# Kernel optimization log

Measured on AMD Instinct MI355X. Metric: run time of the kernel, lower is better.

Reference implementation:

```python
import jax, jax.numpy as jnp
import numpy as np

N = 50000      # nodes
E = 800000     # edges (avg degree 16)
C_IN = 64
C_OUT = 64
H = 32         # hidden_nf (hard-coded in module)
L = 4          # egnn_clean.EGNN default n_layers


def _lin(key, fan_in, fan_out):
    s = 1.0 / np.sqrt(fan_in)
    kw, kb = jax.random.split(key)
    w = jax.random.uniform(kw, (fan_in, fan_out), jnp.float32, -s, s)
    b = jax.random.uniform(kb, (fan_out,), jnp.float32, -s, s)
    return w, b


def _stack(key, fan_in, fan_out):
    ws, bs = zip(*[_lin(jax.random.fold_in(key, l), fan_in, fan_out) for l in range(L)])
    return jnp.stack(ws), jnp.stack(bs)


def setup_inputs() -> dict:
    key = jax.random.key(0)
    k = jax.random.split(key, 16)
    inp = {
        'data': jax.random.normal(k[0], (N, C_IN), jnp.float32),
        'pos': jax.random.normal(k[1], (N, 2), jnp.float32),
        'edge_attr': jax.random.normal(k[2], (E, 1), jnp.float32),
        't': jnp.ones((1,), jnp.float32),
        'row': jax.random.randint(k[3], (E,), 0, N),
        'col': jax.random.randint(k[4], (E,), 0, N),
    }
    inp['emb_in_w'], inp['emb_in_b'] = _lin(k[5], C_IN + 1, H)
    inp['emb_out_w'], inp['emb_out_b'] = _lin(k[6], H, C_OUT)
    inp['edge_w1'], inp['edge_b1'] = _stack(k[7], 2 * H + 2, H)  # [h_i, h_j, radial, edge_attr]
    inp['edge_w2'], inp['edge_b2'] = _stack(k[8], H, H)
    inp['node_w1'], inp['node_b1'] = _stack(k[9], 2 * H, H)
    inp['node_w2'], inp['node_b2'] = _stack(k[10], H, H)
    inp['coord_w1'], inp['coord_b1'] = _stack(k[11], H, H)
    lim = 0.001 * np.sqrt(6.0 / (H + 1))  # xavier_uniform gain=0.001, no bias
    inp['coord_w2'] = jax.random.uniform(k[12], (L, H, 1), jnp.float32, -lim, lim)
    return inp


def _egnn(data, pos, edge_attr, t, emb_in_w, emb_in_b, edge_w1, edge_b1, edge_w2, edge_b2,
          node_w1, node_b1, node_w2, node_b2, coord_w1, coord_b1, coord_w2,
          emb_out_w, emb_out_b, row, col):
    n = data.shape[0]
    silu = jax.nn.silu
    # prepend time channel; pad 2D coords with a zero z-column
    h = jnp.concatenate([jnp.broadcast_to(t.reshape(1, 1), (n, 1)), data], axis=1)  # [N, C_IN+1]
    x = jnp.concatenate([pos, jnp.zeros((n, 1), pos.dtype)], axis=1)                # [N, 3]
    h = h @ emb_in_w + emb_in_b                                                     # [N, H]
    ones_e = jnp.ones((row.shape[0], 1), x.dtype)
    cnt = jnp.maximum(jax.ops.segment_sum(ones_e, row, num_segments=n), 1.0)        # [N,1] clamp(min=1)
    for l in range(L):
        diff = x[row] - x[col]                                    # [E, 3]
        radial = jnp.sum(diff * diff, axis=1, keepdims=True)      # [E, 1]
        ein = jnp.concatenate([h[row], h[col], radial, edge_attr], axis=1)  # [E, 2H+2]
        m = silu(silu(ein @ edge_w1[l] + edge_b1[l]) @ edge_w2[l] + edge_b2[l])  # edge MLP [E, H]
        # equivariant coordinate update (coords_agg='mean')
        phi = silu(m @ coord_w1[l] + coord_b1[l]) @ coord_w2[l]   # [E, 1]
        x = x + jax.ops.segment_sum(diff * phi, row, num_segments=n) / cnt
        # node update (sum aggregation, residual)
        agg = jax.ops.segment_sum(m, row, num_segments=n)         # [N, H]
        upd = silu(jnp.concatenate([h, agg], axis=1) @ node_w1[l] + node_b1[l]) @ node_w2[l] + node_b2[l]
        h = h + upd
    return h @ emb_out_w + emb_out_b                              # [N, C_OUT]


def reference(data, pos, edge_attr, t, emb_in_w, emb_in_b, edge_w1, edge_b1, edge_w2, edge_b2,
              node_w1, node_b1, node_w2, node_b2, coord_w1, coord_b1, coord_w2,
              emb_out_w, emb_out_b, row, col):
    return _egnn(data, pos, edge_attr, t, emb_in_w, emb_in_b, edge_w1, edge_b1, edge_w2, edge_b2,
                 node_w1, node_b1, node_w2, node_b2, coord_w1, coord_b1, coord_w2,
                 emb_out_w, emb_out_b, row, col)
```

## Files before the change

kernel.cpp:

```cpp
#include <hip/hip_runtime.h>
#include <hip/hip_fp16.h>

#define NN 50000
#define NE 800000
#define CIN 64
#define COUT 64
#define HD 32
#define NL 4
#define NB_SCAN 49

typedef float f32x4 __attribute__((ext_vector_type(4)));
typedef _Float16 half8 __attribute__((ext_vector_type(8)));

__device__ __forceinline__ float silu_f(float v) {
    return v * __builtin_amdgcn_rcpf(1.0f + __expf(-v));
}

__global__ __launch_bounds__(256) void embed_kernel(
    const float* __restrict__ data, const float* __restrict__ pos,
    const float* __restrict__ tptr,
    const float* __restrict__ W, const float* __restrict__ b,
    const float* __restrict__ eW1_0,
    float* __restrict__ h, float* __restrict__ x4,
    __half* __restrict__ Hrh, __half* __restrict__ Hch,
    int* __restrict__ cursor, float* __restrict__ aggM, float* __restrict__ aggX4)
{
    int n = blockIdx.x * 256 + threadIdx.x;
    if (n >= NN) return;
    float t = tptr[0];
    float d[CIN];
    const float4* dp = (const float4*)(data + (size_t)n * CIN);
#pragma unroll
    for (int i = 0; i < CIN / 4; i++) {
        float4 v = dp[i];
        d[4*i+0] = v.x; d[4*i+1] = v.y; d[4*i+2] = v.z; d[4*i+3] = v.w;
    }
    float acc[HD];
#pragma unroll
    for (int j = 0; j < HD; j++) acc[j] = fmaf(t, W[j], b[j]);
#pragma unroll
    for (int i = 0; i < CIN; i++) {
        float a = d[i];
#pragma unroll
        for (int j = 0; j < HD; j++) acc[j] = fmaf(a, W[(i + 1) * HD + j], acc[j]);
    }
    float4* hp = (float4*)(h + (size_t)n * HD);
#pragma unroll
    for (int j = 0; j < HD / 4; j++)
        hp[j] = make_float4(acc[4*j], acc[4*j+1], acc[4*j+2], acc[4*j+3]);
    ((float4*)x4)[n] = make_float4(pos[n*2+0], pos[n*2+1], 0.0f, 0.0f);

    float a1[HD], a2[HD];
#pragma unroll
    for (int j = 0; j < HD; j++) { a1[j] = 0.0f; a2[j] = 0.0f; }
#pragma unroll
    for (int i = 0; i < HD; i++) {
        float z = acc[i];
#pragma unroll
        for (int j = 0; j < HD; j++) {
            a1[j] = fmaf(z, eW1_0[i * HD + j], a1[j]);
            a2[j] = fmaf(z, eW1_0[(HD + i) * HD + j], a2[j]);
        }
    }
    int w1[16], w2[16];
#pragma unroll
    for (int q = 0; q < 16; q++) {
        __half2 p1 = __floats2half2_rn(a1[2*q], a1[2*q+1]);
        __half2 p2 = __floats2half2_rn(a2[2*q], a2[2*q+1]);
        w1[q] = *(int*)&p1;
        w2[q] = *(int*)&p2;
    }
    int4* rp = (int4*)(Hrh + (size_t)n * HD);
    int4* cp = (int4*)(Hch + (size_t)n * HD);
#pragma unroll
    for (int q = 0; q < 4; q++) {
        rp[q] = make_int4(w1[4*q], w1[4*q+1], w1[4*q+2], w1[4*q+3]);
        cp[q] = make_int4(w2[4*q], w2[4*q+1], w2[4*q+2], w2[4*q+3]);
    }

    cursor[n] = 0;
    float4 z4 = make_float4(0.f, 0.f, 0.f, 0.f);
    float4* za = (float4*)(aggM + (size_t)n * HD);
#pragma unroll
    for (int j = 0; j < HD/4; j++) za[j] = z4;
    ((float4*)aggX4)[n] = z4;
}

__global__ __launch_bounds__(128) void prep_kernel(
    const float* __restrict__ eW2, const float* __restrict__ cW1,
    __half* __restrict__ w2B, __half* __restrict__ cW1B)
{
    int l  = blockIdx.x;
    int nt = threadIdx.x >> 6;
    int wl = threadIdx.x & 63;
    int rsel = wl & 15, ksel = wl >> 4;
#pragma unroll
    for (int e = 0; e < 8; e++) {
        int k = 8 * ksel + e;
        int j = 16 * nt + rsel;
        size_t o = ((size_t)(l * 2 + nt) * 64 + wl) * 8 + e;
        w2B[o]  = __float2half(eW2[(size_t)l * HD * HD + k * HD + j]);
        cW1B[o] = __float2half(cW1[(size_t)l * HD * HD + k * HD + j]);
    }
}

__global__ __launch_bounds__(256) void hist_kernel(const int* __restrict__ row,
                                                   int* __restrict__ cnt)
{
    int e = blockIdx.x * 256 + threadIdx.x;
    if (e < NE) atomicAdd(&cnt[row[e]], 1);
}

__global__ __launch_bounds__(1024) void scanA_kernel(const int* __restrict__ cnt,
                                                     int* __restrict__ rowstart,
                                                     int* __restrict__ bsum)
{
    __shared__ int sd[1024];
    int i = blockIdx.x * 1024 + threadIdx.x;
    int v = (i < NN) ? cnt[i] : 0;
    sd[threadIdx.x] = v;
    __syncthreads();
    for (int off = 1; off < 1024; off <<= 1) {
        int t = (threadIdx.x >= (unsigned)off) ? sd[threadIdx.x - off] : 0;
        __syncthreads();
        sd[threadIdx.x] += t;
        __syncthreads();
    }
    if (i < NN) rowstart[i] = sd[threadIdx.x] - v;
    if (threadIdx.x == 1023) bsum[blockIdx.x] = sd[1023];
}

__global__ __launch_bounds__(1024) void scanC_kernel(int* __restrict__ rowstart,
                                                     const int* __restrict__ bsum,
                                                     int* __restrict__ cursor)
{
    __shared__ int sb[64];
    if (threadIdx.x < 64) {
        int lane = threadIdx.x;
        int v = (lane < NB_SCAN) ? bsum[lane] : 0;
        int x = v;
        for (int off = 1; off < 64; off <<= 1) {
            int y = __shfl_up(x, off);
            if (lane >= off) x += y;
        }
        sb[lane] = x - v;
        if (lane == 63) rowstart[NN] = x;
    }
    __syncthreads();
    int i = blockIdx.x * 1024 + threadIdx.x;
    if (i < NN) {
        rowstart[i] += sb[blockIdx.x];
        cursor[i] = 0;
    }
}

__global__ __launch_bounds__(256) void scatter_kernel(
    const int* __restrict__ row, const int* __restrict__ col,
    const float* __restrict__ edge_attr,
    const int* __restrict__ rowstart, int* __restrict__ cursor,
    int4* __restrict__ sedge)
{
    int e = blockIdx.x * 256 + threadIdx.x;
    if (e >= NE) return;
    int r = row[e];
    int p = rowstart[r] + atomicAdd(&cursor[r], 1);
    sedge[p] = make_int4(r, col[e], __float_as_int(edge_attr[e]), 0);
}

__global__ __launch_bounds__(256) void edge_fused_kernel(
    const float* __restrict__ x4,
    const int4* __restrict__ sedge,
    const __half* __restrict__ Hrh, const __half* __restrict__ Hch,
    const float* __restrict__ eW1, const float* __restrict__ eb1,
    const float* __restrict__ eb2,
    const __half* __restrict__ w2Bl, const __half* __restrict__ cW1Bl,
    const float* __restrict__ cb1, const float* __restrict__ cW2,
    const int* __restrict__ rowstart,
    float* __restrict__ aggM, float* __restrict__ aggX4)
{
    __shared__ __align__(16) __half At[256][40];
    __shared__ __half sx[256][4];
    __shared__ float  phib[256];
    __shared__ int snf, snl;
    int tid = threadIdx.x;
    int s_base = blockIdx.x * 256;
    int s = s_base + tid;
    int4 ei = sedge[s];
    int r = ei.x, c = ei.y;
    float ea = __int_as_float(ei.z);
    if (tid == 0)   snf = r;
    if (tid == 255) snl = r;

    float4 xr = ((const float4*)x4)[r];
    float4 xc = ((const float4*)x4)[c];
    float d0 = xr.x - xc.x, d1 = xr.y - xc.y, d2 = xr.z - xc.z;
    float radial = d0*d0 + d1*d1 + d2*d2;

    const half8* hr8 = (const half8*)(Hrh + (size_t)r * HD);
    const half8* hc8 = (const half8*)(Hch + (size_t)c * HD);
    int wbuf[16];
#pragma unroll
    for (int i = 0; i < 4; i++) {
        half8 s8 = hr8[i] + hc8[i];
#pragma unroll
        for (int k = 0; k < 8; k += 2) {
            int j = 8*i + k;
            float v0 = (float)s8[k]   + eb1[j]   + radial * eW1[64*HD+j]   + ea * eW1[65*HD+j];
            float v1 = (float)s8[k+1] + eb1[j+1] + radial * eW1[64*HD+j+1] + ea * eW1[65*HD+j+1];
            __half2 p = __floats2half2_rn(silu_f(v0), silu_f(v1));
            wbuf[(j >> 1)] = *(int*)&p;
        }
    }
    int4* arow = (int4*)&At[tid][0];
#pragma unroll
    for (int q = 0; q < 4; q++)
        arow[q] = make_int4(wbuf[4*q], wbuf[4*q+1], wbuf[4*q+2], wbuf[4*q+3]);

    int wl = tid & 63;
    int wbase = tid & 192;
    int rsel = wl & 15, ksel = wl >> 4;

    half8 bw0 = ((const half8*)w2Bl)[wl];
    half8 bw1 = ((const half8*)w2Bl)[64 + wl];
    float bc0 = eb2[rsel], bc1 = eb2[16 + rsel];
    f32x4 acc[4][2];
#pragma unroll
    for (int mt = 0; mt < 4; mt++) {
        acc[mt][0] = (f32x4){bc0, bc0, bc0, bc0};
        acc[mt][1] = (f32x4){bc1, bc1, bc1, bc1};
    }
#pragma unroll
    for (int mt = 0; mt < 4; mt++) {
        half8 af = *(const half8*)&At[wbase + 16*mt + rsel][8*ksel];
        acc[mt][0] = __builtin_amdgcn_mfma_f32_16x16x32_f16(af, bw0, acc[mt][0], 0, 0, 0);
        acc[mt][1] = __builtin_amdgcn_mfma_f32_16x16x32_f16(af, bw1, acc[mt][1], 0, 0, 0);
    }
#pragma unroll
    for (int mt = 0; mt < 4; mt++)
#pragma unroll
        for (int nt = 0; nt < 2; nt++)
#pragma unroll
            for (int q = 0; q < 4; q++) {
                float mv = silu_f(acc[mt][nt][q]);
                At[wbase + 16*mt + 4*ksel + q][16*nt + rsel] = __float2half(mv);
            }

    half8 cw0 = ((const half8*)cW1Bl)[wl];
    half8 cw1 = ((const half8*)cW1Bl)[64 + wl];
    float cc0 = cb1[rsel], cc1 = cb1[16 + rsel];
    f32x4 cacc[4][2];
#pragma unroll
    for (int mt = 0; mt < 4; mt++) {
        cacc[mt][0] = (f32x4){cc0, cc0, cc0, cc0};
        cacc[mt][1] = (f32x4){cc1, cc1, cc1, cc1};
    }
#pragma unroll
    for (int mt = 0; mt < 4; mt++) {
        half8 am = *(const half8*)&At[wbase + 16*mt + rsel][8*ksel];
        cacc[mt][0] = __builtin_amdgcn_mfma_f32_16x16x32_f16(am, cw0, cacc[mt][0], 0, 0, 0);
        cacc[mt][1] = __builtin_amdgcn_mfma_f32_16x16x32_f16(am, cw1, cacc[mt][1], 0, 0, 0);
    }

    float cw2a = cW2[rsel], cw2b = cW2[16 + rsel];
    float p[4][4];
#pragma unroll
    for (int mt = 0; mt < 4; mt++)
#pragma unroll
        for (int q = 0; q < 4; q++)
            p[mt][q] = silu_f(cacc[mt][0][q]) * cw2a + silu_f(cacc[mt][1][q]) * cw2b;
#pragma unroll
    for (int dd = 1; dd < 16; dd <<= 1)
#pragma unroll
        for (int mt = 0; mt < 4; mt++)
#pragma unroll
            for (int q = 0; q < 4; q++)
                p[mt][q] += __shfl_xor(p[mt][q], dd);
    if (rsel == 0) {
#pragma unroll
        for (int mt = 0; mt < 4; mt++)
#pragma unroll
            for (int q = 0; q < 4; q++)
                phib[wbase + 16*mt + 4*ksel + q] = p[mt][q];
    }
    float phi = phib[tid];

    *(__half2*)&sx[tid][0] = __floats2half2_rn(d0 * phi, d1 * phi);
    sx[tid][2] = __float2half(d2 * phi);
    __syncthreads();

    int g = tid >> 5, ch = tid & 31;
    int nf = snf, nl = snl;
    for (int node = nf + g; node <= nl; node += 8) {
        int lo = rowstart[node], hi = rowstart[node + 1];
        int clo = lo - s_base; if (clo < 0) clo = 0;
        int chi = hi - s_base; if (chi > 256) chi = 256;
        if (chi <= clo) continue;
        float am = 0.0f;
        for (int j = clo; j < chi; j++) am += __half2float(At[j][ch]);
        bool interior = (lo >= s_base) && (hi <= s_base + 256);
        if (interior) aggM[(size_t)node * HD + ch] = am;
        else          atomicAdd(&aggM[(size_t)node * HD + ch], am);
        if (ch < 3) {
            float ax = 0.0f;
            for (int j = clo; j < chi; j++) ax += __half2float(sx[j][ch]);
            if (interior) aggX4[(size_t)node * 4 + ch] = ax;
            else          atomicAdd(&aggX4[(size_t)node * 4 + ch], ax);
        }
    }
}

__global__ __launch_bounds__(256) void node_fused_kernel(
    float* __restrict__ h, float* __restrict__ x4,
    float* __restrict__ aggM, float* __restrict__ aggX4,
    const int* __restrict__ rowstart,
    const float* __restrict__ nW1, const float* __restrict__ nb1,
    const float* __restrict__ nW2, const float* __restrict__ nb2,
    const float* __restrict__ eW1n,
    __half* __restrict__ Hrh, __half* __restrict__ Hch,
    const float* __restrict__ Wout, const float* __restrict__ bout,
    float* __restrict__ out)
{
    __shared__ float sIn[8][2*HD];
    __shared__ float sU[8][HD];
    __shared__ float sH[8][HD];
    int local = threadIdx.x >> 5;
    int ch    = threadIdx.x & 31;
    int n = blockIdx.x * 8 + local;
    float hv = h[(size_t)n * HD + ch];
    float am = aggM[(size_t)n * HD + ch];
    aggM[(size_t)n * HD + ch] = 0.0f;
    sIn[local][ch]      = hv;
    sIn[local][HD + ch] = am;
    if (ch < 3) {
        int cnt = rowstart[n + 1] - rowstart[n];
        float cf = (cnt < 1) ? 1.0f : (float)cnt;
        x4[(size_t)n * 4 + ch] += aggX4[(size_t)n * 4 + ch] / cf;
        aggX4[(size_t)n * 4 + ch] = 0.0f;
    }
    __syncthreads();
    float u1 = nb1[ch];
#pragma unroll 8
    for (int i = 0; i < 2*HD; i++) u1 = fmaf(sIn[local][i], nW1[i * HD + ch], u1);
    u1 = silu_f(u1);
    sU[local][ch] = u1;
    __syncthreads();
    float u2 = nb2[ch];
#pragma unroll 8
    for (int i = 0; i < HD; i++) u2 = fmaf(sU[local][i], nW2[i * HD + ch], u2);
    float hn = hv + u2;

    if (eW1n != nullptr) {
        h[(size_t)n * HD + ch] = hn;
        sH[local][ch] = hn;
        __syncthreads();
        float a = 0.0f, b = 0.0f;
#pragma unroll 8
        for (int i = 0; i < HD; i++) {
            float z = sH[local][i];
            a = fmaf(z, eW1n[i * HD + ch], a);
            b = fmaf(z, eW1n[(HD + i) * HD + ch], b);
        }
        Hrh[(size_t)n * HD + ch] = __float2half(a);
        Hch[(size_t)n * HD + ch] = __float2half(b);
    } else {
        sH[local][ch] = hn;
        __syncthreads();
        float o0 = bout[ch], o1 = bout[HD + ch];
#pragma unroll 8
        for (int i = 0; i < HD; i++) {
            float z = sH[local][i];
            o0 = fmaf(z, Wout[i * COUT + ch], o0);
            o1 = fmaf(z, Wout[i * COUT + HD + ch], o1);
        }
        out[(size_t)n * COUT + ch]      = o0;
        out[(size_t)n * COUT + HD + ch] = o1;
    }
}

extern "C" void kernel_launch(void* const* d_in, const int* in_sizes, int n_in,
                              void* d_out, int out_size, void* d_ws, size_t ws_size,
                              hipStream_t stream) {
    const float* data      = (const float*)d_in[0];
    const float* pos       = (const float*)d_in[1];
    const float* edge_attr = (const float*)d_in[2];
    const float* tptr      = (const float*)d_in[3];
    const int*   row       = (const int*)d_in[4];
    const int*   col       = (const int*)d_in[5];
    const float* emb_in_w  = (const float*)d_in[6];
    const float* emb_in_b  = (const float*)d_in[7];
    const float* emb_out_w = (const float*)d_in[8];
    const float* emb_out_b = (const float*)d_in[9];
    const float* edge_w1   = (const float*)d_in[10];
    const float* edge_b1   = (const float*)d_in[11];
    const float* edge_w2   = (const float*)d_in[12];
    const float* edge_b2   = (const float*)d_in[13];
    const float* node_w1   = (const float*)d_in[14];
    const float* node_b1   = (const float*)d_in[15];
    const float* node_w2   = (const float*)d_in[16];
    const float* node_b2   = (const float*)d_in[17];
    const float* coord_w1  = (const float*)d_in[18];
    const float* coord_b1  = (const float*)d_in[19];
    const float* coord_w2  = (const float*)d_in[20];
    float* out = (float*)d_out;

    float* ws = (float*)d_ws;
    float* h      = ws;
    float* x4     = ws + 1600000;
    __half* Hrh   = (__half*)(ws + 1800000);
    __half* Hch   = (__half*)(ws + 2600000);
    float* aggM   = ws + 3400000;
    float* aggX4  = ws + 5000000;
    int* rowstart = (int*)(ws + 5200000);
    int* cursor   = (int*)(ws + 5250004);
    int4* sedge   = (int4*)(ws + 5400000);
    int* bsum     = (int*)(ws + 8600000);
    __half* w2B   = (__half*)(ws + 8600100);
    __half* cW1B  = w2B + (size_t)NL * 1024;

    embed_kernel<<<(NN + 255) / 256, 256, 0, stream>>>(
        data, pos, tptr, emb_in_w, emb_in_b, edge_w1 ,
        h, x4, Hrh, Hch, cursor, aggM, aggX4);
    prep_kernel<<<NL, 128, 0, stream>>>(edge_w2, coord_w1, w2B, cW1B);
    hist_kernel<<<NE / 256, 256, 0, stream>>>(row, cursor);
    scanA_kernel<<<NB_SCAN, 1024, 0, stream>>>(cursor, rowstart, bsum);
    scanC_kernel<<<NB_SCAN, 1024, 0, stream>>>(rowstart, bsum, cursor);
    scatter_kernel<<<NE / 256, 256, 0, stream>>>(row, col, edge_attr, rowstart, cursor, sedge);

    for (int l = 0; l < NL; l++) {
        edge_fused_kernel<<<NE / 256, 256, 0, stream>>>(
            x4, sedge, Hrh, Hch,
            edge_w1 + l * (2*HD+2) * HD, edge_b1 + l * HD,
            edge_b2 + l * HD,
            w2B + (size_t)l * 1024, cW1B + (size_t)l * 1024,
            coord_b1 + l * HD, coord_w2 + l * HD,
            rowstart, aggM, aggX4);
        bool lastl = (l + 1 == NL);
        node_fused_kernel<<<NN / 8, 256, 0, stream>>>(
            h, x4, aggM, aggX4, rowstart,
            node_w1 + l * 2 * HD * HD, node_b1 + l * HD,
            node_w2 + l * HD * HD,     node_b2 + l * HD,
            lastl ? nullptr : (edge_w1 + (l + 1) * (2*HD+2) * HD), Hrh, Hch,
            emb_out_w, emb_out_b, lastl ? out : nullptr);
    }
}
```

Measured before the change: 458.9 us.

## Replace global-atomic counting sort with two-level LDS bucket sort of edges

The per-node histogram, two-kernel scan and global-atomic scatter are replaced by a two-pass radix-style sort. Edges are first bucketed by row>>8 using shared-memory staging, then each bucket is sorted by node inside LDS and written back coalesced. This removes 800k contended global atomics and scattered 16-byte writes, and it makes edge order within a row deterministic per block. The cost is an extra temporary edge buffer pass and a fixed MAXB shared-memory cap that assumes no bucket exceeds 4864 edges.

Measured after the change: 419.7 us. -8.5%, faster.

```diff
diff --git a/kernel.cpp b/kernel.cpp
--- a/kernel.cpp
+++ b/kernel.cpp
@@ -7,7 +7,10 @@
 #define COUT 64
 #define HD 32
 #define NL 4
-#define NB_SCAN 49
+#define NBUK 196
+#define BUKSH 8
+#define EPB 3125
+#define MAXB 4864
 
 typedef float f32x4 __attribute__((ext_vector_type(4)));
 typedef _Float16 half8 __attribute__((ext_vector_type(8)));
@@ -23,7 +26,7 @@
     const float* __restrict__ eW1_0,
     float* __restrict__ h, float* __restrict__ x4,
     __half* __restrict__ Hrh, __half* __restrict__ Hch,
-    int* __restrict__ cursor, float* __restrict__ aggM, float* __restrict__ aggX4)
+    int* __restrict__ bcnt, float* __restrict__ aggM, float* __restrict__ aggX4)
 {
     int n = blockIdx.x * 256 + threadIdx.x;
     if (n >= NN) return;
@@ -78,7 +81,7 @@
         cp[q] = make_int4(w2[4*q], w2[4*q+1], w2[4*q+2], w2[4*q+3]);
     }
 
-    cursor[n] = 0;
+    if (n < NBUK) bcnt[n] = 0;
     float4 z4 = make_float4(0.f, 0.f, 0.f, 0.f);
     float4* za = (float4*)(aggM + (size_t)n * HD);
 #pragma unroll
@@ -104,67 +107,126 @@
     }
 }
 
-__global__ __launch_bounds__(256) void hist_kernel(const int* __restrict__ row,
-                                                   int* __restrict__ cnt)
-{
-    int e = blockIdx.x * 256 + threadIdx.x;
-    if (e < NE) atomicAdd(&cnt[row[e]], 1);
-}
-
-__global__ __launch_bounds__(1024) void scanA_kernel(const int* __restrict__ cnt,
-                                                     int* __restrict__ rowstart,
-                                                     int* __restrict__ bsum)
-{
-    __shared__ int sd[1024];
-    int i = blockIdx.x * 1024 + threadIdx.x;
-    int v = (i < NN) ? cnt[i] : 0;
-    sd[threadIdx.x] = v;
-    __syncthreads();
-    for (int off = 1; off < 1024; off <<= 1) {
-        int t = (threadIdx.x >= (unsigned)off) ? sd[threadIdx.x - off] : 0;
-        __syncthreads();
-        sd[threadIdx.x] += t;
-        __syncthreads();
-    }
-    if (i < NN) rowstart[i] = sd[threadIdx.x] - v;
-    if (threadIdx.x == 1023) bsum[blockIdx.x] = sd[1023];
-}
-
-__global__ __launch_bounds__(1024) void scanC_kernel(int* __restrict__ rowstart,
-                                                     const int* __restrict__ bsum,
-                                                     int* __restrict__ cursor)
-{
-    __shared__ int sb[64];
-    if (threadIdx.x < 64) {
-        int lane = threadIdx.x;
-        int v = (lane < NB_SCAN) ? bsum[lane] : 0;
-        int x = v;
-        for (int off = 1; off < 64; off <<= 1) {
-            int y = __shfl_up(x, off);
-            if (lane >= off) x += y;
-        }
-        sb[lane] = x - v;
-        if (lane == 63) rowstart[NN] = x;
-    }
-    __syncthreads();
-    int i = blockIdx.x * 1024 + threadIdx.x;
-    if (i < NN) {
-        rowstart[i] += sb[blockIdx.x];
-        cursor[i] = 0;
-    }
-}
-
-__global__ __launch_bounds__(256) void scatter_kernel(
+__global__ __launch_bounds__(256) void sortS1_kernel(
+    const int* __restrict__ row, int* __restrict__ bcnt, int* __restrict__ resv)
+{
+    __shared__ int lb[256];
+    int tid = threadIdx.x;
+    lb[tid] = 0;
+    __syncthreads();
+    int base = blockIdx.x * EPB;
+    for (int i = tid; i < EPB; i += 256)
+        atomicAdd(&lb[row[base + i] >> BUKSH], 1);
+    __syncthreads();
+    if (tid < NBUK)
+        resv[blockIdx.x * NBUK + tid] = atomicAdd(&bcnt[tid], lb[tid]);
+}
+
+__global__ __launch_bounds__(256) void sortS2_kernel(
+    const int* __restrict__ bcnt, int* __restrict__ bbase)
+{
+    __shared__ int sd[256];
+    int tid = threadIdx.x;
+    int v = (tid < NBUK) ? bcnt[tid] : 0;
+    sd[tid] = v;
+    __syncthreads();
+    for (int off = 1; off < 256; off <<= 1) {
+        int t = (tid >= off) ? sd[tid - off] : 0;
+        __syncthreads();
+        sd[tid] += t;
+        __syncthreads();
+    }
+    if (tid < NBUK) bbase[tid] = sd[tid] - v;
+    if (tid == 255) bbase[NBUK] = sd[255];
+}
+
+__global__ __launch_bounds__(256) void sortS3_kernel(
     const int* __restrict__ row, const int* __restrict__ col,
-    const float* __restrict__ edge_attr,
-    const int* __restrict__ rowstart, int* __restrict__ cursor,
-    int4* __restrict__ sedge)
-{
-    int e = blockIdx.x * 256 + threadIdx.x;
-    if (e >= NE) return;
-    int r = row[e];
-    int p = rowstart[r] + atomicAdd(&cursor[r], 1);
-    sedge[p] = make_int4(r, col[e], __float_as_int(edge_attr[e]), 0);
+    const float* __restrict__ eattr,
+    const int* __restrict__ bbase, const int* __restrict__ resv,
+    int4* __restrict__ tmp)
+{
+    __shared__ int4 st[EPB];
+    __shared__ int lb[256];
+    __shared__ int lbex[NBUK];
+    __shared__ int lcur[NBUK];
+    __shared__ int sd[256];
+    int tid = threadIdx.x;
+    int base = blockIdx.x * EPB;
+    lb[tid] = 0;
+    if (tid < NBUK) lcur[tid] = 0;
+    __syncthreads();
+    for (int i = tid; i < EPB; i += 256)
+        atomicAdd(&lb[row[base + i] >> BUKSH], 1);
+    __syncthreads();
+    int v = lb[tid];
+    sd[tid] = v;
+    __syncthreads();
+    for (int off = 1; off < 256; off <<= 1) {
+        int t = (tid >= off) ? sd[tid - off] : 0;
+        __syncthreads();
+        sd[tid] += t;
+        __syncthreads();
+    }
+    if (tid < NBUK) lbex[tid] = sd[tid] - v;
+    __syncthreads();
+    for (int i = tid; i < EPB; i += 256) {
+        int e = base + i;
+        int r = row[e];
+        int b = r >> BUKSH;
+        int p = lbex[b] + atomicAdd(&lcur[b], 1);
+        st[p] = make_int4(r, col[e], __float_as_int(eattr[e]), 0);
+    }
+    __syncthreads();
+    int wid = tid >> 6, lane = tid & 63;
+    for (int k = wid; k < NBUK; k += 4) {
+        int L = lb[k];
+        int g = bbase[k] + resv[blockIdx.x * NBUK + k];
+        int o = lbex[k];
+        for (int i = lane; i < L; i += 64)
+            tmp[g + i] = st[o + i];
+    }
+}
+
+__global__ __launch_bounds__(256) void sortS4_kernel(
+    const int4* __restrict__ tmp, const int* __restrict__ bbase,
+    int4* __restrict__ sedge, int* __restrict__ rowstart)
+{
+    __shared__ int4 st[MAXB];
+    __shared__ int lcnt[256], lex[256], lcur[256], sd[256];
+    int tid = threadIdx.x;
+    int k = blockIdx.x;
+    int lo = bbase[k], hi = bbase[k + 1];
+    int nE = hi - lo;
+    int nodeBase = k << BUKSH;
+    lcnt[tid] = 0; lcur[tid] = 0;
+    __syncthreads();
+    for (int i = tid; i < nE; i += 256)
+        atomicAdd(&lcnt[tmp[lo + i].x - nodeBase], 1);
+    __syncthreads();
+    int v = lcnt[tid];
+    sd[tid] = v;
+    __syncthreads();
+    for (int off = 1; off < 256; off <<= 1) {
+        int t = (tid >= off) ? sd[tid - off] : 0;
+        __syncthreads();
+        sd[tid] += t;
+        __syncthreads();
+    }
+    lex[tid] = sd[tid] - v;
+    int n = nodeBase + tid;
+    if (n < NN) rowstart[n] = lo + lex[tid];
+    if (k == NBUK - 1 && tid == 0) rowstart[NN] = NE;
+    __syncthreads();
+    for (int i = tid; i < nE; i += 256) {
+        int4 e = tmp[lo + i];
+        int ln = e.x - nodeBase;
+        int p = lex[ln] + atomicAdd(&lcur[ln], 1);
+        st[p] = e;
+    }
+    __syncthreads();
+    for (int i = tid; i < nE; i += 256)
+        sedge[lo + i] = st[i];
 }
 
 __global__ __launch_bounds__(256) void edge_fused_kernel(
@@ -203,10 +265,10 @@
     for (int i = 0; i < 4; i++) {
         half8 s8 = hr8[i] + hc8[i];
 #pragma unroll
-        for (int k = 0; k < 8; k += 2) {
-            int j = 8*i + k;
-            float v0 = (float)s8[k]   + eb1[j]   + radial * eW1[64*HD+j]   + ea * eW1[65*HD+j];
-            float v1 = (float)s8[k+1] + eb1[j+1] + radial * eW1[64*HD+j+1] + ea * eW1[65*HD+j+1];
+        for (int kk = 0; kk < 8; kk += 2) {
+            int j = 8*i + kk;
+            float v0 = (float)s8[kk]   + eb1[j]   + radial * eW1[64*HD+j]   + ea * eW1[65*HD+j];
+            float v1 = (float)s8[kk+1] + eb1[j+1] + radial * eW1[64*HD+j+1] + ea * eW1[65*HD+j+1];
             __half2 p = __floats2half2_rn(silu_f(v0), silu_f(v1));
             wbuf[(j >> 1)] = *(int*)&p;
         }
@@ -411,20 +473,22 @@
     float* aggM   = ws + 3400000;
     float* aggX4  = ws + 5000000;
     int* rowstart = (int*)(ws + 5200000);
-    int* cursor   = (int*)(ws + 5250004);
+    int* bcnt     = (int*)(ws + 5250004);
+    int* bbase    = (int*)(ws + 5250204);
+    int* resv     = (int*)(ws + 5250404);
     int4* sedge   = (int4*)(ws + 5400000);
-    int* bsum     = (int*)(ws + 8600000);
-    __half* w2B   = (__half*)(ws + 8600100);
+    int4* tmp     = (int4*)(ws + 8600000);
+    __half* w2B   = (__half*)(ws + 11800000);
     __half* cW1B  = w2B + (size_t)NL * 1024;
 
     embed_kernel<<<(NN + 255) / 256, 256, 0, stream>>>(
         data, pos, tptr, emb_in_w, emb_in_b, edge_w1 ,
-        h, x4, Hrh, Hch, cursor, aggM, aggX4);
+        h, x4, Hrh, Hch, bcnt, aggM, aggX4);
     prep_kernel<<<NL, 128, 0, stream>>>(edge_w2, coord_w1, w2B, cW1B);
-    hist_kernel<<<NE / 256, 256, 0, stream>>>(row, cursor);
-    scanA_kernel<<<NB_SCAN, 1024, 0, stream>>>(cursor, rowstart, bsum);
-    scanC_kernel<<<NB_SCAN, 1024, 0, stream>>>(rowstart, bsum, cursor);
-    scatter_kernel<<<NE / 256, 256, 0, stream>>>(row, col, edge_attr, rowstart, cursor, sedge);
+    sortS1_kernel<<<256, 256, 0, stream>>>(row, bcnt, resv);
+    sortS2_kernel<<<1, 256, 0, stream>>>(bcnt, bbase);
+    sortS3_kernel<<<256, 256, 0, stream>>>(row, col, edge_attr, bbase, resv, tmp);
+    sortS4_kernel<<<NBUK, 256, 0, stream>>>(tmp, bbase, sedge, rowstart);
 
     for (int l = 0; l < NL; l++) {
         edge_fused_kernel<<<NE / 256, 256, 0, stream>>>(
```
